# Optimization experiments

Measured on AMD Instinct MI355X. Metric: run time of the kernel, lower is better.

Reference implementation:

```python
import jax, jax.numpy as jnp
import numpy as np

N, H, E, K = 256, 128, 64, 4  # nodes, hidden, dist-embed dim, heads
ALPHA = 0.2  # leaky-relu slope


def setup_inputs() -> dict:
    key = jax.random.key(0)
    ks = jax.random.split(key, 12)
    s = lambda k, sh: (jax.random.normal(k, sh, jnp.float32) * 0.05)
    return dict(
        action_hidden_state=jax.random.normal(ks[0], (N, H), jnp.float32),
        goal_hidden_state=jax.random.normal(ks[1], (N, H), jnp.float32),
        goal=jax.random.normal(ks[2], (N, 2), jnp.float32),
        action=jax.random.normal(ks[3], (N, 2), jnp.float32),
        W_emb=s(ks[4], (1, E)), b_emb=jnp.zeros((E,), jnp.float32),
        W_gate=s(ks[5], (2 * E + 2 * H, H)), b_gate=jnp.zeros((H,), jnp.float32),
        W_gat=s(ks[6], (K, H, H)), a_src=s(ks[7], (K, H)), a_dst=s(ks[8], (K, H)),
        gat_bias=jnp.zeros((H,), jnp.float32),
    )


def cal_dist(goal, action):
    # Vectorized, math-faithful (incl. source typos) version of the O(n^2) loop.
    ax, ay = action[:, 0], action[:, 1]
    gx, gy = goal[:, 0], goal[:, 1]
    a1x, a1y = ax[:, None], ay[:, None]   # node i
    a2x, a2y = ax[None, :], ay[None, :]   # node j
    g1x, g1y = gx[:, None], gy[:, None]
    g2x, g2y = gx[None, :], gy[None, :]
    dn = (a1x - a1x) * (g1y - g2y) - (a1y - a2y) * (g1x - g2x)
    cross_a = a1x * a2y - a1y * a2x
    gterm = g1x * g2y - g1x * g2x
    n1 = cross_a * (g1x - g2x) - (a1x - a2x) * gterm
    n2 = cross_a * (g1y - g2y) - (a1y - a2x) * gterm
    safe = jnp.where(dn == 0.0, 1.0, dn)
    p1, p2 = n1 / safe, n2 / safe
    base = jnp.linalg.norm(action - goal, axis=-1)  # [n]
    d1p = jnp.sqrt((a1x - p1) ** 2 + (a1y - p2) ** 2)
    d2p = jnp.sqrt((a2x - p1) ** 2 + (a2y - p2) ** 2)
    cond = (dn != 0.0) & ((a1x - p1) * (p1 - g1x) > 0.0)
    ones = jnp.ones_like(dn)
    d1 = jnp.where(cond, d1p, base[:, None] * ones)
    d2 = jnp.where(cond, d2p, base[None, :] * ones)
    n = d1.shape[0]
    ii = jnp.arange(n)[:, None]
    jj = jnp.arange(n)[None, :]
    # dist[i,j]=d1(i,j) for i<j; dist[j,i]=d2(i,j) i.e. lower triangle = d2.T; diag = |a_i - g_i|
    return jnp.where(ii == jj, base[:, None] * ones, jnp.where(ii < jj, d1, d2.T))


def reference(action_hidden_state, goal_hidden_state, goal, action,
              W_emb, b_emb, W_gate, b_gate, W_gat, a_src, a_dst, gat_bias):
    ha, hg = action_hidden_state, goal_hidden_state
    n, h = ha.shape
    dist = cal_dist(goal, action)                      # [n,n]
    emb = dist[..., None] * W_emb[0] + b_emb           # Linear(1,E) -> [n,n,E]
    # pairwise interaction gate (i != idx branch, computed for all pairs)
    gate_in = jnp.concatenate([
        jnp.broadcast_to(ha[:, None, :], (n, n, h)),
        jnp.broadcast_to(ha[None, :, :], (n, n, h)),
        emb, jnp.swapaxes(emb, 0, 1)], axis=-1)        # [n,n,2H+2E]
    gate = jax.nn.sigmoid(gate_in @ W_gate + b_gate)   # [n,n,H]
    gated = ha[None, :, :] * gate
    # self branch: gates the goal hidden state; action row stays ungated
    emb_d = emb[jnp.arange(n), jnp.arange(n)]          # [n,E]
    gate_self = jax.nn.sigmoid(
        jnp.concatenate([ha, hg, emb_d, emb_d], axis=-1) @ W_gate + b_gate)
    curr_goal = hg * gate_self                         # [n,H]
    eye = jnp.eye(n, dtype=bool)[..., None]
    curr_action = jnp.where(eye, ha[:, None, :], gated)          # [n,n,H]
    gat_in = jnp.concatenate([curr_action, curr_goal[:, None, :]], axis=1)  # [n,n+1,H]
    # multi-head GAT layer (batched over the n query nodes)
    hp = jnp.einsum('bmf,kfo->bkmo', gat_in, W_gat)    # [n,K,m,H]
    attn = (jnp.einsum('bkmo,ko->bkm', hp, a_src)[..., :, None]
            + jnp.einsum('bkmo,ko->bkm', hp, a_dst)[..., None, :])  # [n,K,m,m]
    attn = jax.nn.softmax(jax.nn.leaky_relu(attn, ALPHA), axis=-1)
    out = jnp.einsum('bkij,bkjo->bkio', attn, hp).mean(axis=1) + gat_bias  # [n,m,H]
    out = jax.nn.elu(out)
    idx = jnp.arange(n)
    return out[idx, idx]                               # [n,H]
```

## Files before the change

kernel.cpp:

```cpp
#include <hip/hip_runtime.h>
#include <math.h>

#define N 256
#define H 128
#define E 64
#define K 4
#define M (N + 1)
#define WAVES 16
#define BLOCK 1024

__device__ __forceinline__ float sigm(float x) {
    return __fdividef(1.0f, 1.0f + __expf(-x));
}

__device__ __forceinline__ float wave_sum(float v) {
#pragma unroll
    for (int d = 1; d < 64; d <<= 1) v += __shfl_xor(v, d, 64);
    return v;
}

__device__ __forceinline__ float readlane_f(float v, int l) {
    return __uint_as_float(__builtin_amdgcn_readlane(__float_as_uint(v), l));
}

__device__ __forceinline__ float kbutterfly(float q0, float q1, float q2, float q3,
                                            int lane) {
    const bool b1 = lane & 1;
    const bool b2 = lane & 2;
    float aA = b1 ? q1 : q0, aB = b1 ? q0 : q1;
    aA += __shfl_xor(aB, 1, 64);
    float cA = b1 ? q3 : q2, cB = b1 ? q2 : q3;
    cA += __shfl_xor(cB, 1, 64);
    float eA = b2 ? cA : aA, eB = b2 ? aA : cA;
    eA += __shfl_xor(eB, 2, 64);
#pragma unroll
    for (int d = 4; d < 64; d <<= 1) eA += __shfl_xor(eA, d, 64);
    return eA;
}

__device__ __forceinline__ float base_of(float2 a, float2 g) {
    float dx = __fsub_rn(a.x, g.x), dy = __fsub_rn(a.y, g.y);
    return __fsqrt_rn(__fadd_rn(__fmul_rn(dx, dx), __fmul_rn(dy, dy)));
}

__device__ __forceinline__ void pairdist(
    float a1x, float a1y, float a2x, float a2y,
    float g1x, float g1y, float g2x, float g2y,
    float baseR, float baseC, float& d_rc, float& d_cr)
{
    float t  = __fmul_rn(__fsub_rn(a1y, a2y), __fsub_rn(g1x, g2x));
    float dn = -t;
    float ca = __fsub_rn(__fmul_rn(a1x, a2y), __fmul_rn(a1y, a2x));
    float gt = __fsub_rn(__fmul_rn(g1x, g2y), __fmul_rn(g1x, g2x));
    float n1 = __fsub_rn(__fmul_rn(ca, __fsub_rn(g1x, g2x)),
                         __fmul_rn(__fsub_rn(a1x, a2x), gt));
    float n2 = __fsub_rn(__fmul_rn(ca, __fsub_rn(g1y, g2y)),
                         __fmul_rn(__fsub_rn(a1y, a2x), gt));
    float safe = (dn == 0.0f) ? 1.0f : dn;
    float p1 = __fdiv_rn(n1, safe);
    float p2 = __fdiv_rn(n2, safe);
    bool cond = (dn != 0.0f) &&
                (__fmul_rn(__fsub_rn(a1x, p1), __fsub_rn(p1, g1x)) > 0.0f);
    float dx1 = __fsub_rn(a1x, p1), dy1 = __fsub_rn(a1y, p2);
    float d1p = __fsqrt_rn(__fadd_rn(__fmul_rn(dx1, dx1), __fmul_rn(dy1, dy1)));
    float dx2 = __fsub_rn(a2x, p1), dy2 = __fsub_rn(a2y, p2);
    float d2p = __fsqrt_rn(__fadd_rn(__fmul_rn(dx2, dx2), __fmul_rn(dy2, dy2)));
    d_rc = cond ? d1p : baseR;
    d_cr = cond ? d2p : baseC;
}

__global__ __launch_bounds__(BLOCK) void gat_pre(
    const float* __restrict__ ha, const float* __restrict__ hg,
    const float* __restrict__ W_emb, const float* __restrict__ b_emb,
    const float* __restrict__ W_gate, const float* __restrict__ b_gate,
    const float* __restrict__ W_gat, const float* __restrict__ a_src,
    const float* __restrict__ a_dst,
    float* __restrict__ A1, float* __restrict__ G2,
    float* __restrict__ u3g, float* __restrict__ u4g, float* __restrict__ ccg,
    float* __restrict__ vsrc, float* __restrict__ vdst,
    float4* __restrict__ pk)
{
    const int b    = blockIdx.x;
    const int tid  = threadIdx.x;
    const int wid  = tid >> 6;
    const int lane = tid & 63;

    __shared__ float sRed[8][3][H];
    __shared__ float sA2[H];
    __shared__ float sU[8][3][64];

    {
        const int f  = tid & (H - 1);
        const int sl = tid >> 7;
        const int g0 = sl * 16;
        float s1 = 0.f, s2 = 0.f, s3 = 0.f;
#pragma unroll
        for (int g = 0; g < 16; ++g) {
            const int gg = g0 + g;
            float w1 = W_gate[gg * H + f];
            float w2 = W_gate[(H + gg) * H + f];
            float av = ha[b * H + gg];
            float gv = hg[b * H + gg];
            s1 += av * w1;
            s2 += av * w2;
            s3 += gv * w2;
        }
        sRed[sl][0][f] = s1;
        sRed[sl][1][f] = s2;
        sRed[sl][2][f] = s3;
    }

    if (wid >= 14) {
        const int p = 2 * b + (wid - 14);
        const int k = p >> 7;
        const int f = p & (H - 1);
        const float2 w2 = ((const float2*)&W_gat[(k * H + f) * H])[lane];
        const float2 as2 = ((const float2*)&a_src[k * H])[lane];
        const float2 ad2 = ((const float2*)&a_dst[k * H])[lane];
        float vsv = wave_sum(w2.x * as2.x + w2.y * as2.y);
        float vdv = wave_sum(w2.x * ad2.x + w2.y * ad2.y);
        if (lane == 0) { vsrc[k * H + f] = vsv; vdst[k * H + f] = vdv; }
    }

    if (b < 2 && wid >= 2 && wid < 10) {
        const int sl = wid - 2;
        const int f  = (b << 6) | lane;
        float s3 = 0.f, s4 = 0.f, scc = 0.f;
#pragma unroll
        for (int e0 = 0; e0 < 8; ++e0) {
            const int e = sl * 8 + e0;
            float w3 = W_gate[(2 * H + e) * H + f];
            float w4 = W_gate[(2 * H + E + e) * H + f];
            float we = W_emb[e], be = b_emb[e];
            s3  += we * w3;
            s4  += we * w4;
            scc += be * (w3 + w4);
        }
        sU[sl][0][lane] = s3;
        sU[sl][1][lane] = s4;
        sU[sl][2][lane] = scc;
    }
    __syncthreads();

    if (tid < 3 * H) {
        const int c = tid >> 7;
        const int f = tid & (H - 1);
        float r = 0.f;
#pragma unroll
        for (int sl = 0; sl < 8; ++sl) r += sRed[sl][c][f];
        if (c == 0)      A1[b * H + f] = r;
        else if (c == 2) G2[b * H + f] = r;
        else             sA2[f] = r;
    }
    __syncthreads();

    if (tid < 64) {
        const float2 h2 = ((const float2*)&ha[b * H])[tid];
        pk[(b << 6) | tid] = make_float4(sA2[2 * tid], sA2[2 * tid + 1], h2.x, h2.y);
    }
    if (b < 2 && tid < 192) {
        const int c  = tid >> 6;
        const int fl = tid & 63;
        float r = 0.f;
#pragma unroll
        for (int w = 0; w < 8; ++w) r += sU[w][c][fl];
        const int f = (b << 6) | fl;
        if (c == 0)      u3g[f] = r;
        else if (c == 1) u4g[f] = r;
        else             ccg[f] = r + b_gate[f];
    }
}

__global__ __launch_bounds__(BLOCK) void gat_main(
    const float* __restrict__ ha, const float* __restrict__ hg,
    const float* __restrict__ W_gat, const float* __restrict__ gat_bias,
    const float* __restrict__ A1, const float* __restrict__ G2,
    const float* __restrict__ u3a, const float* __restrict__ u4a,
    const float* __restrict__ cca,
    const float* __restrict__ vsrc, const float* __restrict__ vdst,
    const float4* __restrict__ pk,
    const float* __restrict__ goal, const float* __restrict__ action,
    float* __restrict__ out)
{
    const int i    = blockIdx.x;
    const int tid  = threadIdx.x;
    const int wid  = tid >> 6;
    const int lane = tid & 63;
    const int f0   = lane * 2;

    __shared__ float sW[WAVES][K][H];
    __shared__ float sL[WAVES][K];
    __shared__ float sWfin[K][H];
    __shared__ float sPart[8][H];

    const float2 a1v = *(const float2*)&A1[i * H + f0];
    const float2 haI = *(const float2*)&ha[i * H + f0];
    const float2 hgI = *(const float2*)&hg[i * H + f0];
    const float2 g2v = *(const float2*)&G2[i * H + f0];
    const float2 u3  = *(const float2*)&u3a[f0];
    const float2 u4  = *(const float2*)&u4a[f0];
    const float2 cc  = *(const float2*)&cca[f0];
    const float2 vd0 = *(const float2*)&vdst[0 * H + f0];
    const float2 vd1 = *(const float2*)&vdst[1 * H + f0];
    const float2 vd2 = *(const float2*)&vdst[2 * H + f0];
    const float2 vd3 = *(const float2*)&vdst[3 * H + f0];
    const float2 vs0 = *(const float2*)&vsrc[0 * H + f0];
    const float2 vs1 = *(const float2*)&vsrc[1 * H + f0];
    const float2 vs2 = *(const float2*)&vsrc[2 * H + f0];
    const float2 vs3 = *(const float2*)&vsrc[3 * H + f0];

    float dijv = 0.f, djiv = 0.f;
    if (lane < 16) {
        const int j = wid + 16 * lane;
        if (j != i) {
            const float2 aI = ((const float2*)action)[i];
            const float2 gI = ((const float2*)goal)[i];
            const float2 aJ = ((const float2*)action)[j];
            const float2 gJ = ((const float2*)goal)[j];
            const float bI = base_of(aI, gI);
            const float bJ = base_of(aJ, gJ);
            if (i < j)
                pairdist(aI.x, aI.y, aJ.x, aJ.y, gI.x, gI.y, gJ.x, gJ.y,
                         bI, bJ, dijv, djiv);
            else
                pairdist(aJ.x, aJ.y, aI.x, aI.y, gJ.x, gJ.y, gI.x, gI.y,
                         bJ, bI, djiv, dijv);
        }
    }

    const float scOwn = kbutterfly(haI.x * vs0.x + haI.y * vs0.y,
                                   haI.x * vs1.x + haI.y * vs1.y,
                                   haI.x * vs2.x + haI.y * vs2.y,
                                   haI.x * vs3.x + haI.y * vs3.y, lane);

    const float2 a1cc = make_float2(a1v.x + cc.x, a1v.y + cc.y);

    float l_ = 0.f;
    float w00 = 0.f, w01 = 0.f, w02 = 0.f, w03 = 0.f;
    float w10 = 0.f, w11 = 0.f, w12 = 0.f, w13 = 0.f;

#pragma unroll
    for (int t = 0; t < 16; ++t) {
        const int jj = wid + 16 * t;
        const float4 ph = pk[(jj << 6) | lane];
        const float dx = readlane_f(dijv, t);
        const float dy = readlane_f(djiv, t);
        float tx = a1cc.x + ph.x + dx * u3.x + dy * u4.x;
        float ty = a1cc.y + ph.y + dx * u3.y + dy * u4.y;
        float2 g = make_float2(ph.z * sigm(tx), ph.w * sigm(ty));
        if (jj == i) g = haI;

        float q0 = g.x * vd0.x + g.y * vd0.y;
        float q1 = g.x * vd1.x + g.y * vd1.y;
        float q2 = g.x * vd2.x + g.y * vd2.y;
        float q3 = g.x * vd3.x + g.y * vd3.y;
        float e  = kbutterfly(q0, q1, q2, q3, lane);

        float lg = scOwn + e;
        lg = (lg >= 0.f) ? lg : 0.2f * lg;
        const float p = __expf(lg);
        l_ += p;

        const float p0 = readlane_f(p, 0), p1 = readlane_f(p, 1);
        const float p2 = readlane_f(p, 2), p3 = readlane_f(p, 3);
        w00 += p0 * g.x;  w10 += p0 * g.y;
        w01 += p1 * g.x;  w11 += p1 * g.y;
        w02 += p2 * g.x;  w12 += p2 * g.y;
        w03 += p3 * g.x;  w13 += p3 * g.y;
    }

    if (wid == 0) {
        const float2 aI = ((const float2*)action)[i];
        const float2 gI = ((const float2*)goal)[i];
        const float baseI = base_of(aI, gI);
        float tx = a1cc.x + g2v.x + baseI * (u3.x + u4.x);
        float ty = a1cc.y + g2v.y + baseI * (u3.y + u4.y);
        float2 g = make_float2(hgI.x * sigm(tx), hgI.y * sigm(ty));

        float q0 = g.x * vd0.x + g.y * vd0.y;
        float q1 = g.x * vd1.x + g.y * vd1.y;
        float q2 = g.x * vd2.x + g.y * vd2.y;
        float q3 = g.x * vd3.x + g.y * vd3.y;
        float e  = kbutterfly(q0, q1, q2, q3, lane);

        float lg = scOwn + e;
        lg = (lg >= 0.f) ? lg : 0.2f * lg;
        const float p = __expf(lg);
        l_ += p;

        const float p0 = readlane_f(p, 0), p1 = readlane_f(p, 1);
        const float p2 = readlane_f(p, 2), p3 = readlane_f(p, 3);
        w00 += p0 * g.x;  w10 += p0 * g.y;
        w01 += p1 * g.x;  w11 += p1 * g.y;
        w02 += p2 * g.x;  w12 += p2 * g.y;
        w03 += p3 * g.x;  w13 += p3 * g.y;
    }

    *(float2*)&sW[wid][0][f0] = make_float2(w00, w10);
    *(float2*)&sW[wid][1][f0] = make_float2(w01, w11);
    *(float2*)&sW[wid][2][f0] = make_float2(w02, w12);
    *(float2*)&sW[wid][3][f0] = make_float2(w03, w13);
    if (lane < K) sL[wid][lane] = l_;
    __syncthreads();

    if (tid < K * H) {
        const int k = tid >> 7;
        const int f = tid & (H - 1);
        float W = 0.f;
#pragma unroll
        for (int w = 0; w < WAVES; ++w) W += sW[w][k][f];
        float L = 0.f;
#pragma unroll
        for (int w = 0; w < WAVES; ++w) L += sL[w][k];
        sWfin[k][f] = W / L;
    }
    __syncthreads();

    {
        const int f = tid & (H - 1);
        const int s = tid >> 7;
        float acc = 0.0f;
#pragma unroll
        for (int k = 0; k < K; ++k) {
            const int g0 = s * 16;
#pragma unroll
            for (int g = 0; g < 16; ++g)
                acc += sWfin[k][g0 + g] * W_gat[(k * H + g0 + g) * H + f];
        }
        sPart[s][f] = acc;
    }
    __syncthreads();

    if (tid < H) {
        float acc = 0.0f;
#pragma unroll
        for (int s = 0; s < 8; ++s) acc += sPart[s][tid];
        float val = 0.25f * acc + gat_bias[tid];
        out[i * H + tid] = (val > 0.0f) ? val : expm1f(val);
    }
}

extern "C" void kernel_launch(void* const* d_in, const int* in_sizes, int n_in,
                              void* d_out, int out_size, void* d_ws, size_t ws_size,
                              hipStream_t stream)
{
    const float* ha       = (const float*)d_in[0];
    const float* hg       = (const float*)d_in[1];
    const float* goal     = (const float*)d_in[2];
    const float* action   = (const float*)d_in[3];
    const float* W_emb    = (const float*)d_in[4];
    const float* b_emb    = (const float*)d_in[5];
    const float* W_gate   = (const float*)d_in[6];
    const float* b_gate   = (const float*)d_in[7];
    const float* W_gat    = (const float*)d_in[8];
    const float* a_src    = (const float*)d_in[9];
    const float* a_dst    = (const float*)d_in[10];
    const float* gat_bias = (const float*)d_in[11];

    float* ws  = (float*)d_ws;
    float*  A1 = ws;
    float*  G2 = A1 + N * H;
    float*  u3 = G2 + N * H;
    float*  u4 = u3 + H;
    float*  cc = u4 + H;
    float*  vs = cc + H;
    float*  vd = vs + K * H;
    float4* pk = (float4*)(vd + K * H);

    hipLaunchKernelGGL(gat_pre, dim3(N), dim3(BLOCK), 0, stream,
                       ha, hg, W_emb, b_emb, W_gate, b_gate,
                       W_gat, a_src, a_dst,
                       A1, G2, u3, u4, cc, vs, vd, pk);

    hipLaunchKernelGGL(gat_main, dim3(N), dim3(BLOCK), 0, stream,
                       ha, hg, W_gat, gat_bias,
                       A1, G2, u3, u4, cc, vs, vd, pk,
                       goal, action, (float*)d_out);
}
```

Before: 26.60 us.

## Halve block sizes: two rows per pre block, 512-thread main blocks

The pre kernel now processes two node rows per 1024-thread block over N/2 blocks. Each thread does two reduction passes, and four waves per block compute the vsrc/vdst projections. The main kernel drops to 8 waves of 512 threads, each wave handling 32 neighbours instead of 16, and the final projection loops twice per thread. This trades less per-block parallelism for fewer, fuller blocks and more co-resident blocks per CU, aiming to cut launch/scheduling and barrier overhead.

```diff
diff --git a/kernel.cpp b/kernel.cpp
--- a/kernel.cpp
+++ b/kernel.cpp
@@ -6,8 +6,9 @@
 #define E 64
 #define K 4
 #define M (N + 1)
-#define WAVES 16
-#define BLOCK 1024
+#define MWAVES 8
+#define MBLOCK 512
+#define PBLOCK 1024
 
 __device__ __forceinline__ float sigm(float x) {
     return __fdividef(1.0f, 1.0f + __expf(-x));
@@ -69,7 +70,7 @@
     d_cr = cond ? d2p : baseC;
 }
 
-__global__ __launch_bounds__(BLOCK) void gat_pre(
+__global__ __launch_bounds__(PBLOCK) void gat_pre(
     const float* __restrict__ ha, const float* __restrict__ hg,
     const float* __restrict__ W_emb, const float* __restrict__ b_emb,
     const float* __restrict__ W_gate, const float* __restrict__ b_gate,
@@ -85,13 +86,19 @@
     const int wid  = tid >> 6;
     const int lane = tid & 63;
 
-    __shared__ float sRed[8][3][H];
-    __shared__ float sA2[H];
+    __shared__ float sRed[2][8][3][H];
+    __shared__ float sA2[2][H];
     __shared__ float sU[8][3][64];
 
-    {
-        const int f  = tid & (H - 1);
-        const int sl = tid >> 7;
+    const int rloc = wid >> 3;
+    const int row  = 2 * b + rloc;
+    const int tir  = tid & 511;
+    const int f    = tir & (H - 1);
+    const int q    = tir >> 7;
+
+#pragma unroll
+    for (int pass = 0; pass < 2; ++pass) {
+        const int sl = q + 4 * pass;
         const int g0 = sl * 16;
         float s1 = 0.f, s2 = 0.f, s3 = 0.f;
 #pragma unroll
@@ -99,38 +106,38 @@
             const int gg = g0 + g;
             float w1 = W_gate[gg * H + f];
             float w2 = W_gate[(H + gg) * H + f];
-            float av = ha[b * H + gg];
-            float gv = hg[b * H + gg];
+            float av = ha[row * H + gg];
+            float gv = hg[row * H + gg];
             s1 += av * w1;
             s2 += av * w2;
             s3 += gv * w2;
         }
-        sRed[sl][0][f] = s1;
-        sRed[sl][1][f] = s2;
-        sRed[sl][2][f] = s3;
-    }
-
-    if (wid >= 14) {
-        const int p = 2 * b + (wid - 14);
-        const int k = p >> 7;
-        const int f = p & (H - 1);
-        const float2 w2 = ((const float2*)&W_gat[(k * H + f) * H])[lane];
+        sRed[rloc][sl][0][f] = s1;
+        sRed[rloc][sl][1][f] = s2;
+        sRed[rloc][sl][2][f] = s3;
+    }
+
+    if (wid >= 12) {
+        const int p  = 4 * b + (wid - 12);
+        const int k  = p >> 7;
+        const int fv = p & (H - 1);
+        const float2 w2  = ((const float2*)&W_gat[(k * H + fv) * H])[lane];
         const float2 as2 = ((const float2*)&a_src[k * H])[lane];
         const float2 ad2 = ((const float2*)&a_dst[k * H])[lane];
         float vsv = wave_sum(w2.x * as2.x + w2.y * as2.y);
         float vdv = wave_sum(w2.x * ad2.x + w2.y * ad2.y);
-        if (lane == 0) { vsrc[k * H + f] = vsv; vdst[k * H + f] = vdv; }
+        if (lane == 0) { vsrc[k * H + fv] = vsv; vdst[k * H + fv] = vdv; }
     }
 
     if (b < 2 && wid >= 2 && wid < 10) {
         const int sl = wid - 2;
-        const int f  = (b << 6) | lane;
+        const int fu = (b << 6) | lane;
         float s3 = 0.f, s4 = 0.f, scc = 0.f;
 #pragma unroll
         for (int e0 = 0; e0 < 8; ++e0) {
             const int e = sl * 8 + e0;
-            float w3 = W_gate[(2 * H + e) * H + f];
-            float w4 = W_gate[(2 * H + E + e) * H + f];
+            float w3 = W_gate[(2 * H + e) * H + fu];
+            float w4 = W_gate[(2 * H + E + e) * H + fu];
             float we = W_emb[e], be = b_emb[e];
             s3  += we * w3;
             s4  += we * w4;
@@ -142,21 +149,28 @@
     }
     __syncthreads();
 
-    if (tid < 3 * H) {
-        const int c = tid >> 7;
-        const int f = tid & (H - 1);
+    if (tid < 768) {
+        const int rl    = (tid >= 384) ? 1 : 0;
+        const int inner = tid - 384 * rl;
+        const int c     = inner >> 7;
+        const int ff    = inner & (H - 1);
         float r = 0.f;
 #pragma unroll
-        for (int sl = 0; sl < 8; ++sl) r += sRed[sl][c][f];
-        if (c == 0)      A1[b * H + f] = r;
-        else if (c == 2) G2[b * H + f] = r;
-        else             sA2[f] = r;
-    }
-    __syncthreads();
-
-    if (tid < 64) {
-        const float2 h2 = ((const float2*)&ha[b * H])[tid];
-        pk[(b << 6) | tid] = make_float4(sA2[2 * tid], sA2[2 * tid + 1], h2.x, h2.y);
+        for (int sl = 0; sl < 8; ++sl) r += sRed[rl][sl][c][ff];
+        const int rw = 2 * b + rl;
+        if (c == 0)      A1[rw * H + ff] = r;
+        else if (c == 2) G2[rw * H + ff] = r;
+        else             sA2[rl][ff] = r;
+    }
+    __syncthreads();
+
+    if (tid < 128) {
+        const int rl  = tid >> 6;
+        const int col = tid & 63;
+        const int rw  = 2 * b + rl;
+        const float2 h2 = ((const float2*)&ha[rw * H])[col];
+        pk[(rw << 6) | col] = make_float4(sA2[rl][2 * col], sA2[rl][2 * col + 1],
+                                          h2.x, h2.y);
     }
     if (b < 2 && tid < 192) {
         const int c  = tid >> 6;
@@ -164,14 +178,14 @@
         float r = 0.f;
 #pragma unroll
         for (int w = 0; w < 8; ++w) r += sU[w][c][fl];
-        const int f = (b << 6) | fl;
-        if (c == 0)      u3g[f] = r;
-        else if (c == 1) u4g[f] = r;
-        else             ccg[f] = r + b_gate[f];
-    }
-}
-
-__global__ __launch_bounds__(BLOCK) void gat_main(
+        const int fu = (b << 6) | fl;
+        if (c == 0)      u3g[fu] = r;
+        else if (c == 1) u4g[fu] = r;
+        else             ccg[fu] = r + b_gate[fu];
+    }
+}
+
+__global__ __launch_bounds__(MBLOCK) void gat_main(
     const float* __restrict__ ha, const float* __restrict__ hg,
     const float* __restrict__ W_gat, const float* __restrict__ gat_bias,
     const float* __restrict__ A1, const float* __restrict__ G2,
@@ -188,8 +202,8 @@
     const int lane = tid & 63;
     const int f0   = lane * 2;
 
-    __shared__ float sW[WAVES][K][H];
-    __shared__ float sL[WAVES][K];
+    __shared__ float sW[MWAVES][K][H];
+    __shared__ float sL[MWAVES][K];
     __shared__ float sWfin[K][H];
     __shared__ float sPart[8][H];
 
@@ -210,8 +224,8 @@
     const float2 vs3 = *(const float2*)&vsrc[3 * H + f0];
 
     float dijv = 0.f, djiv = 0.f;
-    if (lane < 16) {
-        const int j = wid + 16 * lane;
+    if (lane < 32) {
+        const int j = wid + 8 * lane;
         if (j != i) {
             const float2 aI = ((const float2*)action)[i];
             const float2 gI = ((const float2*)goal)[i];
@@ -240,8 +254,8 @@
     float w10 = 0.f, w11 = 0.f, w12 = 0.f, w13 = 0.f;
 
 #pragma unroll
-    for (int t = 0; t < 16; ++t) {
-        const int jj = wid + 16 * t;
+    for (int t = 0; t < 32; ++t) {
+        const int jj = wid + 8 * t;
         const float4 ph = pk[(jj << 6) | lane];
         const float dx = readlane_f(dijv, t);
         const float dy = readlane_f(djiv, t);
@@ -303,31 +317,35 @@
     if (lane < K) sL[wid][lane] = l_;
     __syncthreads();
 
-    if (tid < K * H) {
+    {
         const int k = tid >> 7;
         const int f = tid & (H - 1);
         float W = 0.f;
 #pragma unroll
-        for (int w = 0; w < WAVES; ++w) W += sW[w][k][f];
+        for (int w = 0; w < MWAVES; ++w) W += sW[w][k][f];
         float L = 0.f;
 #pragma unroll
-        for (int w = 0; w < WAVES; ++w) L += sL[w][k];
+        for (int w = 0; w < MWAVES; ++w) L += sL[w][k];
         sWfin[k][f] = W / L;
     }
     __syncthreads();
 
     {
-        const int f = tid & (H - 1);
-        const int s = tid >> 7;
-        float acc = 0.0f;
-#pragma unroll
-        for (int k = 0; k < K; ++k) {
+        const int f  = tid & (H - 1);
+        const int s0 = tid >> 7;
+#pragma unroll
+        for (int pass = 0; pass < 2; ++pass) {
+            const int s  = s0 + 4 * pass;
             const int g0 = s * 16;
-#pragma unroll
-            for (int g = 0; g < 16; ++g)
-                acc += sWfin[k][g0 + g] * W_gat[(k * H + g0 + g) * H + f];
+            float acc = 0.0f;
+#pragma unroll
+            for (int k = 0; k < K; ++k) {
+#pragma unroll
+                for (int g = 0; g < 16; ++g)
+                    acc += sWfin[k][g0 + g] * W_gat[(k * H + g0 + g) * H + f];
+            }
+            sPart[s][f] = acc;
         }
-        sPart[s][f] = acc;
     }
     __syncthreads();
 
@@ -367,12 +385,12 @@
     float*  vd = vs + K * H;
     float4* pk = (float4*)(vd + K * H);
 
-    hipLaunchKernelGGL(gat_pre, dim3(N), dim3(BLOCK), 0, stream,
+    hipLaunchKernelGGL(gat_pre, dim3(N / 2), dim3(PBLOCK), 0, stream,
                        ha, hg, W_emb, b_emb, W_gate, b_gate,
                        W_gat, a_src, a_dst,
                        A1, G2, u3, u4, cc, vs, vd, pk);
 
-    hipLaunchKernelGGL(gat_main, dim3(N), dim3(BLOCK), 0, stream,
+    hipLaunchKernelGGL(gat_main, dim3(N), dim3(MBLOCK), 0, stream,
                        ha, hg, W_gat, gat_bias,
                        A1, G2, u3, u4, cc, vs, vd, pk,
                        goal, action, (float*)d_out);
```

Result: slower. 29.28 us (+10.1%).

## Split main GAT kernel into two half-row blocks plus a separate projection kernel

Applied to the files above, without the earlier changes.

The 1024-thread per-node main kernel becomes two 512-thread blocks per node. Each block covers half of the waves and writes partial attention-weighted sums and softmax denominators to workspace. A third kernel combines the two partials, normalises them, and applies the W_gat projection, bias and ELU. This is meant to raise occupancy and spread work across more CUs, at the cost of an extra kernel launch and a global-memory round trip for the partials.

```diff
diff --git a/kernel.cpp b/kernel.cpp
--- a/kernel.cpp
+++ b/kernel.cpp
@@ -5,9 +5,6 @@
 #define H 128
 #define E 64
 #define K 4
-#define M (N + 1)
-#define WAVES 16
-#define BLOCK 1024
 
 __device__ __forceinline__ float sigm(float x) {
     return __fdividef(1.0f, 1.0f + __expf(-x));
@@ -69,7 +66,7 @@
     d_cr = cond ? d2p : baseC;
 }
 
-__global__ __launch_bounds__(BLOCK) void gat_pre(
+__global__ __launch_bounds__(1024) void gat_pre(
     const float* __restrict__ ha, const float* __restrict__ hg,
     const float* __restrict__ W_emb, const float* __restrict__ b_emb,
     const float* __restrict__ W_gate, const float* __restrict__ b_gate,
@@ -114,7 +111,7 @@
         const int p = 2 * b + (wid - 14);
         const int k = p >> 7;
         const int f = p & (H - 1);
-        const float2 w2 = ((const float2*)&W_gat[(k * H + f) * H])[lane];
+        const float2 w2  = ((const float2*)&W_gat[(k * H + f) * H])[lane];
         const float2 as2 = ((const float2*)&a_src[k * H])[lane];
         const float2 ad2 = ((const float2*)&a_dst[k * H])[lane];
         float vsv = wave_sum(w2.x * as2.x + w2.y * as2.y);
@@ -171,27 +168,28 @@
     }
 }
 
-__global__ __launch_bounds__(BLOCK) void gat_main(
+__global__ __launch_bounds__(512) void gat_main1(
     const float* __restrict__ ha, const float* __restrict__ hg,
-    const float* __restrict__ W_gat, const float* __restrict__ gat_bias,
+    const float* __restrict__ gat_bias,
     const float* __restrict__ A1, const float* __restrict__ G2,
     const float* __restrict__ u3a, const float* __restrict__ u4a,
     const float* __restrict__ cca,
     const float* __restrict__ vsrc, const float* __restrict__ vdst,
     const float4* __restrict__ pk,
     const float* __restrict__ goal, const float* __restrict__ action,
-    float* __restrict__ out)
+    float* __restrict__ Wp, float* __restrict__ Lp)
 {
-    const int i    = blockIdx.x;
+    const int b    = blockIdx.x;
+    const int i    = b >> 1;
+    const int h    = b & 1;
     const int tid  = threadIdx.x;
-    const int wid  = tid >> 6;
+    const int w    = tid >> 6;
+    const int wid  = 8 * h + w;
     const int lane = tid & 63;
     const int f0   = lane * 2;
 
-    __shared__ float sW[WAVES][K][H];
-    __shared__ float sL[WAVES][K];
-    __shared__ float sWfin[K][H];
-    __shared__ float sPart[8][H];
+    __shared__ float sW[8][K][H];
+    __shared__ float sL[8][K];
 
     const float2 a1v = *(const float2*)&A1[i * H + f0];
     const float2 haI = *(const float2*)&ha[i * H + f0];
@@ -296,38 +294,66 @@
         w03 += p3 * g.x;  w13 += p3 * g.y;
     }
 
-    *(float2*)&sW[wid][0][f0] = make_float2(w00, w10);
-    *(float2*)&sW[wid][1][f0] = make_float2(w01, w11);
-    *(float2*)&sW[wid][2][f0] = make_float2(w02, w12);
-    *(float2*)&sW[wid][3][f0] = make_float2(w03, w13);
-    if (lane < K) sL[wid][lane] = l_;
+    *(float2*)&sW[w][0][f0] = make_float2(w00, w10);
+    *(float2*)&sW[w][1][f0] = make_float2(w01, w11);
+    *(float2*)&sW[w][2][f0] = make_float2(w02, w12);
+    *(float2*)&sW[w][3][f0] = make_float2(w03, w13);
+    if (lane < K) sL[w][lane] = l_;
     __syncthreads();
 
-    if (tid < K * H) {
+    {
         const int k = tid >> 7;
         const int f = tid & (H - 1);
-        float W = 0.f;
-#pragma unroll
-        for (int w = 0; w < WAVES; ++w) W += sW[w][k][f];
-        float L = 0.f;
-#pragma unroll
-        for (int w = 0; w < WAVES; ++w) L += sL[w][k];
-        sWfin[k][f] = W / L;
+        float Ws = 0.f;
+#pragma unroll
+        for (int q = 0; q < 8; ++q) Ws += sW[q][k][f];
+        Wp[b * (K * H) + k * H + f] = Ws;
+        if (f == 0) {
+            float Ls = 0.f;
+#pragma unroll
+            for (int q = 0; q < 8; ++q) Ls += sL[q][k];
+            Lp[b * K + k] = Ls;
+        }
+    }
+}
+
+__global__ __launch_bounds__(512) void gat_main2(
+    const float* __restrict__ W_gat, const float* __restrict__ gat_bias,
+    const float* __restrict__ Wp, const float* __restrict__ Lp,
+    float* __restrict__ out)
+{
+    const int i   = blockIdx.x;
+    const int tid = threadIdx.x;
+
+    __shared__ float sWfin[K][H];
+    __shared__ float sPart[8][H];
+
+    {
+        const int k = tid >> 7;
+        const int f = tid & (H - 1);
+        const float Wsum = Wp[(2 * i) * (K * H) + k * H + f] +
+                           Wp[(2 * i + 1) * (K * H) + k * H + f];
+        const float Lsum = Lp[(2 * i) * K + k] + Lp[(2 * i + 1) * K + k];
+        sWfin[k][f] = Wsum / Lsum;
     }
     __syncthreads();
 
     {
-        const int f = tid & (H - 1);
-        const int s = tid >> 7;
-        float acc = 0.0f;
-#pragma unroll
-        for (int k = 0; k < K; ++k) {
+        const int f  = tid & (H - 1);
+        const int s0 = tid >> 7;
+#pragma unroll
+        for (int pass = 0; pass < 2; ++pass) {
+            const int s  = s0 + 4 * pass;
             const int g0 = s * 16;
-#pragma unroll
-            for (int g = 0; g < 16; ++g)
-                acc += sWfin[k][g0 + g] * W_gat[(k * H + g0 + g) * H + f];
+            float acc = 0.0f;
+#pragma unroll
+            for (int k = 0; k < K; ++k) {
+#pragma unroll
+                for (int g = 0; g < 16; ++g)
+                    acc += sWfin[k][g0 + g] * W_gat[(k * H + g0 + g) * H + f];
+            }
+            sPart[s][f] = acc;
         }
-        sPart[s][f] = acc;
     }
     __syncthreads();
 
@@ -366,14 +392,19 @@
     float*  vs = cc + H;
     float*  vd = vs + K * H;
     float4* pk = (float4*)(vd + K * H);
-
-    hipLaunchKernelGGL(gat_pre, dim3(N), dim3(BLOCK), 0, stream,
+    float*  Wp = (float*)(pk + N * 64);
+    float*  Lp = Wp + 512 * K * H;
+
+    hipLaunchKernelGGL(gat_pre, dim3(N), dim3(1024), 0, stream,
                        ha, hg, W_emb, b_emb, W_gate, b_gate,
                        W_gat, a_src, a_dst,
                        A1, G2, u3, u4, cc, vs, vd, pk);
 
-    hipLaunchKernelGGL(gat_main, dim3(N), dim3(BLOCK), 0, stream,
-                       ha, hg, W_gat, gat_bias,
+    hipLaunchKernelGGL(gat_main1, dim3(2 * N), dim3(512), 0, stream,
+                       ha, hg, gat_bias,
                        A1, G2, u3, u4, cc, vs, vd, pk,
-                       goal, action, (float*)d_out);
-}
+                       goal, action, Wp, Lp);
+
+    hipLaunchKernelGGL(gat_main2, dim3(N), dim3(512), 0, stream,
+                       W_gat, gat_bias, Wp, Lp, (float*)d_out);
+}
```

Result: slower. 29.01 us (+9.0%).
